# Kernel tuning notes

Measured on AMD Instinct MI355X. Metric: run time of the kernel, lower is better.

## Reference

```python
import jax, jax.numpy as jnp
import numpy as np

H, N, LMAX, KCH = 128, 64, 256, 2  # d_model, d_state, l_max per axis, kernel channels (bidirectional)


def _ssm_kernel(A_re, A_im, C_re, C_im, log_dt, L):
    """S4D diagonal SSM kernel (ZOH discretization) -> real kernel (KCH, H, L)."""
    A = A_re + 1j * A_im                      # (H, N)
    C = C_re + 1j * C_im                      # (KCH, H, N)
    dt = jnp.exp(log_dt)                      # (H,)
    dtA = dt[:, None] * A                     # (H, N)
    K = C * (jnp.exp(dtA) - 1.0) / A          # (KCH, H, N)
    vand = jnp.exp(dtA[:, :, None] * jnp.arange(L, dtype=dtA.real.dtype))  # (H, N, L)
    return 2.0 * jnp.einsum('chn,hnl->chl', K, vand).real


def _bidir_pad(k, L_in):
    """Split 2 kernel channels into fwd/bwd, flip backward one, pad to length Lk+L_in."""
    k0, k1 = k[:1], k[1:]                     # each (1, H, Lk)
    fwd = jnp.pad(k0, ((0, 0), (0, 0), (0, L_in)))
    bwd = jnp.pad(k1[..., ::-1], ((0, 0), (0, 0), (L_in, 0)))
    return fwd + bwd                          # (1, H, Lk + L_in)


def setup_inputs() -> dict:
    key = jax.random.key(0)
    ks = jax.random.split(key, 8)
    B, L1, L2 = 2, 256, 256
    u = jax.random.normal(ks[0], (B, H, L1, L2), jnp.float32)
    D = jax.random.normal(ks[1], (1, H), jnp.float32)

    def kparams(k_c, k_ci, k_dt):
        A_re = -0.5 * jnp.ones((H, N), jnp.float32)
        A_im = jnp.pi * jnp.broadcast_to(jnp.arange(N, dtype=jnp.float32), (H, N))
        C_re = jax.random.normal(k_c, (KCH, H, N), jnp.float32) * (0.5 ** 0.5)
        C_im = jax.random.normal(k_ci, (KCH, H, N), jnp.float32) * (0.5 ** 0.5)
        log_dt = jax.random.uniform(k_dt, (H,), jnp.float32,
                                    minval=np.log(1e-3), maxval=np.log(1e-1))
        return A_re, A_im, C_re, C_im, log_dt

    A_re0, A_im0, C_re0, C_im0, log_dt0 = kparams(ks[2], ks[3], ks[4])
    A_re1, A_im1, C_re1, C_im1, log_dt1 = kparams(ks[5], ks[6], ks[7])
    return {"u": u, "D": D,
            "A_re0": A_re0, "A_im0": A_im0, "C_re0": C_re0, "C_im0": C_im0, "log_dt0": log_dt0,
            "A_re1": A_re1, "A_im1": A_im1, "C_re1": C_re1, "C_im1": C_im1, "log_dt1": log_dt1}


def reference(u, D, A_re0, A_im0, C_re0, C_im0, log_dt0,
              A_re1, A_im1, C_re1, C_im1, log_dt1):
    B, _, L1, L2 = u.shape
    Lk1, Lk2 = min(L1, LMAX), min(L2, LMAX)
    # per-axis SSM kernels, then bidirectional flip-and-pad
    k1 = _bidir_pad(_ssm_kernel(A_re0, A_im0, C_re0, C_im0, log_dt0, Lk1), L1)  # (1,H,P1)
    k2 = _bidir_pad(_ssm_kernel(A_re1, A_im1, C_re1, C_im1, log_dt1, Lk2), L2)  # (1,H,P2)
    P1, P2 = L1 + Lk1, L2 + Lk2
    # N-D FFT convolution
    u_f = jnp.fft.rfftn(u, s=(P1, P2), axes=(-2, -1))        # (B,H,P1,P2//2+1)
    kf1 = jnp.fft.fft(k1, n=P1, axis=-1)                     # (1,H,P1) complex
    kf2 = jnp.fft.rfft(k2, n=P2, axis=-1)                    # (1,H,P2//2+1)
    k_f = jnp.einsum('chm,chn->chmn', kf1, kf2)              # outer product over axes (trank=1)
    y_f = jnp.einsum('bhmn,chmn->bchmn', u_f, k_f)           # (B,1,H,P1,P2r)
    y = jnp.fft.irfftn(y_f, s=(P1, P2), axes=(-2, -1))[..., :L1, :L2]
    # skip connection D
    y = y + jnp.einsum('bhxy,ch->bchxy', u, D)
    return y.reshape(B, -1, L1, L2)                          # (B, C*H, L1, L2)
```

## Files before the change

kernel.cpp:

```cpp
#include <hip/hip_runtime.h>

#define HH 128
#define NN 64
#define LL 256
#define WP 280

typedef __attribute__((ext_vector_type(8))) short bf8;
typedef __attribute__((ext_vector_type(4))) float f32x4;

__device__ inline ushort f2bf(float f) {
    uint x = __float_as_uint(f);
    return (ushort)((x + 0x7fffu + ((x >> 16) & 1u)) >> 16);
}
__device__ inline uint cvt_pk_bf16(float lo, float hi) {
    uint r;
    asm volatile("v_cvt_pk_bf16_f32 %0, %1, %2" : "=v"(r) : "v"(lo), "v"(hi));
    return r;
}
#define MFMA(a,b,c) __builtin_amdgcn_mfma_f32_16x16x32_bf16((a),(b),(c),0,0,0)

__global__ __launch_bounds__(512) void ssm_gen_fast(
    const float* __restrict__ A_re0, const float* __restrict__ A_im0,
    const float* __restrict__ C_re0, const float* __restrict__ C_im0,
    const float* __restrict__ log_dt0,
    const float* __restrict__ A_re1, const float* __restrict__ A_im1,
    const float* __restrict__ C_re1, const float* __restrict__ C_im1,
    const float* __restrict__ log_dt1,
    uint* __restrict__ arrg)
{
    __shared__ float4 par[128];
    __shared__ float  red[512];
    __shared__ ushort rev[512];

    int tid = threadIdx.x;
    int h   = blockIdx.x;
    int s   = blockIdx.y;

    if (tid < 128) {
        int n  = tid & 63;
        int ch = tid >> 6;
        const float* Ar = s ? A_re1 : A_re0;
        const float* Ai = s ? A_im1 : A_im0;
        const float* Cr = s ? C_re1 : C_re0;
        const float* Ci = s ? C_im1 : C_im0;
        const float* Ld = s ? log_dt1 : log_dt0;
        float dt = __expf(Ld[h]);
        float ar = Ar[h*NN + n], ai = Ai[h*NN + n];
        float cr = Cr[(ch*HH + h)*NN + n], ci = Ci[(ch*HH + h)*NN + n];
        float xr = dt * ar, xi = dt * ai;
        float phr = xi * 0.15915494f;
        float phf = phr - floorf(phr);
        float sn = __sinf(6.2831853f * phf);
        float cs = __cosf(6.2831853f * phf);
        float e  = __expf(xr);
        float er = e*cs - 1.f, ei = e*sn;
        float inv = 1.f / (ar*ar + ai*ai);
        float dr = (er*ar + ei*ai) * inv;
        float di = (ei*ar - er*ai) * inv;
        float Kr = 2.f*(cr*dr - ci*di);
        float Ki = 2.f*(cr*di + ci*dr);
        par[tid] = (float4){ xr, xi * 0.15915494f, Kr, Ki };
    }
    __syncthreads();

    {
        int l  = tid & 255;
        int ch = tid >> 8;
        float lf = (float)l;
#pragma unroll
        for (int nh = 0; nh < 2; ++nh) {
            const float4* pb = &par[ch*64 + nh*32];
            float acc = 0.f;
            for (int n = 0; n < 32; ++n) {
                float4 p = pb[n];
                float mag = __expf(p.x * lf);
                float ph  = p.y * lf;
                float phf = ph - floorf(ph);
                float ang = 6.2831853f * phf;
                acc += p.z * (mag * __cosf(ang)) - p.w * (mag * __sinf(ang));
            }
            if (nh == 0) red[tid] = acc;
            else {
                int ri = ch ? (256 + l) : (255 - l);
                rev[ri] = f2bf(red[tid] + acc);
            }
        }
    }
    __syncthreads();

    {
        int j  = tid & 255;
        uint lo, hi;
        if (tid < 256) { lo = rev[2*j];     hi = rev[2*j + 1]; }
        else           { lo = rev[2*j + 1]; hi = (j == 255) ? 0u : (uint)rev[2*j + 2]; }
        arrg[(s*HH + h)*512 + tid] = lo | (hi << 16);
    }
}

#define GL0(dst, addr)  asm volatile("global_load_dwordx4 %0, %1, off"           : "=v"(dst) : "v"(addr))
#define GL16(dst, addr) asm volatile("global_load_dwordx4 %0, %1, off offset:16" : "=v"(dst) : "v"(addr))
#define VMW(n) do { asm volatile("s_waitcnt vmcnt(" #n ")" ::: "memory"); \
                    __builtin_amdgcn_sched_barrier(0); } while (0)

#define WINROLL8(T, JB, t_)                                                   \
    { int jj = (JB) + 8*(t_); uint* pw = (uint*)&win[(t_) & 7];               \
      pw[0]=T[jj]; pw[1]=T[jj+1]; pw[2]=T[jj+2]; pw[3]=T[jj+3]; }

#define PH1_ISS(kk, N0, N1)                                                   \
    { const float* a_ = rp + (kk)*32 + 8*q; GL0(N0, a_); GL16(N1, a_); }

#define PH1_CON(kk, C0, C1, CNT)                                              \
    {                                                                         \
        if ((kk) > 0) { WINROLL8(T2, jb2, 2*(kk)-1); WINROLL8(T2, jb2, 2*(kk)); } \
        VMW(CNT);                                                             \
        bf8 b0_; uint* pb_ = (uint*)&b0_;                                     \
        pb_[0]=cvt_pk_bf16(C0.x,C0.y); pb_[1]=cvt_pk_bf16(C0.z,C0.w);         \
        pb_[2]=cvt_pk_bf16(C1.x,C1.y); pb_[3]=cvt_pk_bf16(C1.z,C1.w);         \
        __builtin_amdgcn_s_setprio(1);                                        \
        _Pragma("unroll")                                                     \
        for (int mi = 0; mi < 8; ++mi)                                        \
            acc[mi] = MFMA(win[(2*(kk)-mi) & 7], b0_, acc[mi]);               \
        __builtin_amdgcn_s_setprio(0);                                        \
    }

__global__ __launch_bounds__(512, 4) void s4nd_v6(
    const float* __restrict__ u, const float* __restrict__ Dv,
    const uint* __restrict__ arrg, float* __restrict__ out)
{
    __shared__ ushort WT[128 * WP];
    __shared__ uint   arr[2][512];

    int tid = threadIdx.x;
    int j    = blockIdx.x;
    int xcd  = j & 7;
    int k    = j >> 3;
    int bh   = xcd * 32 + (k >> 1);
    int y0   = (k & 1) * 128;
    int h    = bh & (HH - 1);

    arr[0][tid] = arrg[h*512 + tid];
    arr[1][tid] = arrg[(HH + h)*512 + tid];
    __syncthreads();

    int lane = tid & 63;
    int w = tid >> 6;
    int c = lane & 15, q = lane >> 4;
    int wm2 = (w >> 1) * 64, wn2 = (w & 1) * 64;

    const uint* T1 = &arr[0][(c & 1) ? 0 : 256];
    const uint* T2 = &arr[1][(c & 1) ? 0 : 256];
    int jb2 = (255 - y0  - c + 8*q) >> 1;
    int jb1 = (255 - wm2 - c + 8*q) >> 1;

    f32x4 acc[8];
#pragma unroll
    for (int i = 0; i < 8; ++i) acc[i] = (f32x4){0.f,0.f,0.f,0.f};

    const float* ub = u + (size_t)bh * LL * LL;
    float* yb_ = out + (size_t)bh * LL * LL;

#pragma unroll
    for (int ns = 0; ns < 2; ++ns) {
        const float* rp = ub + (size_t)(w*32 + 16*ns + c) * LL;
        bf8 win[8];
#pragma unroll
        for (int t = -7; t <= 0; ++t) WINROLL8(T2, jb2, t);
        float4 S00, S01, S10, S11, S20, S21;
        PH1_ISS(0, S00, S01)
        PH1_ISS(1, S10, S11)
        PH1_ISS(2, S20, S21)  PH1_CON(0, S00, S01, 4)
        PH1_ISS(3, S00, S01)  PH1_CON(1, S10, S11, 4)
        PH1_ISS(4, S10, S11)  PH1_CON(2, S20, S21, 4)
        PH1_ISS(5, S20, S21)  PH1_CON(3, S00, S01, 4)
        PH1_ISS(6, S00, S01)  PH1_CON(4, S10, S11, 4)
        PH1_ISS(7, S10, S11)  PH1_CON(5, S20, S21, 4)
                              PH1_CON(6, S00, S01, 2)
                              PH1_CON(7, S10, S11, 0)
#pragma unroll
        for (int mi = 0; mi < 8; ++mi)
#pragma unroll
            for (int r = 0; r < 4; ++r) {
                int row = 16*mi + 4*q + r;
                WT[row*WP + w*32 + 16*ns + c] = f2bf(acc[mi][r]);
                acc[mi][r] = 0.f;
            }
    }
    __syncthreads();

    float dh = Dv[h];
#pragma unroll
    for (int p = 0; p < 2; ++p) {
        int nb = wn2 + p*32;

        float uh[32];
#pragma unroll
        for (int mi = 0; mi < 4; ++mi)
#pragma unroll
            for (int r = 0; r < 4; ++r) {
                int row = wm2 + 16*mi + 4*q + r;
#pragma unroll
                for (int ni = 0; ni < 2; ++ni)
                    uh[(mi*4 + r)*2 + ni] = ub[(size_t)row*LL + y0 + nb + 16*ni + c];
            }

        bf8 win2[4];
#pragma unroll
        for (int t = -3; t <= 0; ++t) {
            int jj = jb1 + 8*t;
            uint* pw = (uint*)&win2[t & 3];
            pw[0]=T1[jj]; pw[1]=T1[jj+1]; pw[2]=T1[jj+2]; pw[3]=T1[jj+3];
        }
#pragma unroll
        for (int kk = 0; kk < 8; ++kk) {
            if (kk) {
#pragma unroll
                for (int t = 2*kk - 1; t <= 2*kk; ++t) {
                    int jj = jb1 + 8*t;
                    uint* pw = (uint*)&win2[t & 3];
                    pw[0]=T1[jj]; pw[1]=T1[jj+1]; pw[2]=T1[jj+2]; pw[3]=T1[jj+3];
                }
            }
            int xb = kk*32 + 8*q;
            bf8 b0 = *(const bf8*)&WT[(nb + c)*WP + xb];
            bf8 b1 = *(const bf8*)&WT[(nb + 16 + c)*WP + xb];
            __builtin_amdgcn_s_setprio(1);
#pragma unroll
            for (int mi = 0; mi < 4; ++mi) {
                bf8 a = win2[(2*kk - mi) & 3];
                acc[mi*2 + 0] = MFMA(a, b0, acc[mi*2 + 0]);
                acc[mi*2 + 1] = MFMA(a, b1, acc[mi*2 + 1]);
            }
            __builtin_amdgcn_s_setprio(0);
        }

#pragma unroll
        for (int mi = 0; mi < 4; ++mi)
#pragma unroll
            for (int ni = 0; ni < 2; ++ni)
#pragma unroll
                for (int r = 0; r < 4; ++r) {
                    int row = wm2 + 16*mi + 4*q + r;
                    int col = y0 + nb + 16*ni + c;
                    yb_[(size_t)row*LL + col] =
                        acc[mi*2 + ni][r] + dh * uh[(mi*4 + r)*2 + ni];
                    acc[mi*2 + ni][r] = 0.f;
                }
    }
}

extern "C" void kernel_launch(void* const* d_in, const int* in_sizes, int n_in,
                              void* d_out, int out_size, void* d_ws, size_t ws_size,
                              hipStream_t stream)
{
    const float* u       = (const float*)d_in[0];
    const float* D       = (const float*)d_in[1];
    const float* A_re0   = (const float*)d_in[2];
    const float* A_im0   = (const float*)d_in[3];
    const float* C_re0   = (const float*)d_in[4];
    const float* C_im0   = (const float*)d_in[5];
    const float* log_dt0 = (const float*)d_in[6];
    const float* A_re1   = (const float*)d_in[7];
    const float* A_im1   = (const float*)d_in[8];
    const float* C_re1   = (const float*)d_in[9];
    const float* C_im1   = (const float*)d_in[10];
    const float* log_dt1 = (const float*)d_in[11];
    float* out = (float*)d_out;

    uint* arrg = (uint*)d_ws;

    ssm_gen_fast<<<dim3(HH, 2), 512, 0, stream>>>(
        A_re0, A_im0, C_re0, C_im0, log_dt0,
        A_re1, A_im1, C_re1, C_im1, log_dt1, arrg);
    s4nd_v6<<<512, 512, 0, stream>>>(u, D, arrg, out);
}
```

Measured before the change: 49.56 us.

## Pipeline separable convolution passes in k-chunks with double-buffered LDS slices

Restructures the two-pass separable Toeplitz convolution so the first pass (along y) is computed chunk by chunk in 32-row slices and fed through a small double-buffered LDS tile into the second pass, interleaving global loads, first-pass MFMAs and second-pass MFMAs. Each block now covers a 64-column quarter instead of a 128-column half, doubling the grid to 1024 blocks and shrinking LDS from a full 128x280 tile to two 64x40 tiles. The aim is to overlap memory latency with compute and raise occupancy. In exchange it adds eight block-wide barriers per block and recomputes the first pass per y-quarter, which increases the redundant u reads and MFMA work.

```diff
diff --git a/kernel.cpp b/kernel.cpp
--- a/kernel.cpp
+++ b/kernel.cpp
@@ -3,7 +3,7 @@
 #define HH 128
 #define NN 64
 #define LL 256
-#define WP 280
+#define WCP 40
 
 typedef __attribute__((ext_vector_type(8))) short bf8;
 typedef __attribute__((ext_vector_type(4))) float f32x4;
@@ -102,40 +102,68 @@
 #define VMW(n) do { asm volatile("s_waitcnt vmcnt(" #n ")" ::: "memory"); \
                     __builtin_amdgcn_sched_barrier(0); } while (0)
 
-#define WINROLL8(T, JB, t_)                                                   \
-    { int jj = (JB) + 8*(t_); uint* pw = (uint*)&win[(t_) & 7];               \
-      pw[0]=T[jj]; pw[1]=T[jj+1]; pw[2]=T[jj+2]; pw[3]=T[jj+3]; }
-
-#define PH1_ISS(kk, N0, N1)                                                   \
-    { const float* a_ = rp + (kk)*32 + 8*q; GL0(N0, a_); GL16(N1, a_); }
-
-#define PH1_CON(kk, C0, C1, CNT)                                              \
+#define PISS(kc, ys, N0, N1) \
+    { const float* a_ = rpP + (kc)*8192 + (ys)*32 + 8*q; GL0(N0, a_); GL16(N1, a_); }
+
+#define PCON(ys, C0, C1, CNT, APX)                                            \
     {                                                                         \
-        if ((kk) > 0) { WINROLL8(T2, jb2, 2*(kk)-1); WINROLL8(T2, jb2, 2*(kk)); } \
+        int jj = jbP + 16*(ys);                                               \
+        bf8 aF; uint* pa = (uint*)&aF;                                        \
+        pa[0]=T2[jj]; pa[1]=T2[jj+1]; pa[2]=T2[jj+2]; pa[3]=T2[jj+3];         \
         VMW(CNT);                                                             \
-        bf8 b0_; uint* pb_ = (uint*)&b0_;                                     \
-        pb_[0]=cvt_pk_bf16(C0.x,C0.y); pb_[1]=cvt_pk_bf16(C0.z,C0.w);         \
-        pb_[2]=cvt_pk_bf16(C1.x,C1.y); pb_[3]=cvt_pk_bf16(C1.z,C1.w);         \
-        __builtin_amdgcn_s_setprio(1);                                        \
+        bf8 bB; uint* pb = (uint*)&bB;                                        \
+        pb[0]=cvt_pk_bf16(C0.x,C0.y); pb[1]=cvt_pk_bf16(C0.z,C0.w);           \
+        pb[2]=cvt_pk_bf16(C1.x,C1.y); pb[3]=cvt_pk_bf16(C1.z,C1.w);           \
+        APX = MFMA(aF, bB, APX);                                              \
+    }
+
+#define CSLICE(k, ys)                                                         \
+    {                                                                         \
+        if (((ys) & 1) == 0)                                                  \
+            bC = *(const bf8*)&Wc[(k)&1][(16*((ys)>>1) + c)*WCP + 8*q];       \
+        acc2[((ys)&1)*4 + ((ys)>>1)] =                                        \
+            MFMA(win2[(2*(k) - ((ys)&1)) & 3], bC, acc2[((ys)&1)*4 + ((ys)>>1)]); \
+    }
+
+#define WROLL(t_)                                                             \
+    { int jj = jb1 + 8*(t_); uint* pw = (uint*)&win2[(t_) & 3];               \
+      pw[0]=T1[jj]; pw[1]=T1[jj+1]; pw[2]=T1[jj+2]; pw[3]=T1[jj+3]; }
+
+#define BODY(k)                                                               \
+    {                                                                         \
+        WROLL(2*(k)-1) WROLL(2*(k))                                           \
+        bf8 bC;                                                               \
+        PISS((k)+1, 0, P0, P1)                                                \
+        PISS((k)+1, 1, Q0, Q1)  CSLICE(k,0)  PCON(0, P0, P1, 2, accpA)        \
+        PISS((k)+1, 2, P0, P1)  CSLICE(k,1)  PCON(1, Q0, Q1, 2, accpB)        \
+        PISS((k)+1, 3, Q0, Q1)  CSLICE(k,2)  PCON(2, P0, P1, 2, accpA)        \
+        PISS((k)+1, 4, P0, P1)  CSLICE(k,3)  PCON(3, Q0, Q1, 2, accpB)        \
+        PISS((k)+1, 5, Q0, Q1)  CSLICE(k,4)  PCON(4, P0, P1, 2, accpA)        \
+        PISS((k)+1, 6, P0, P1)  CSLICE(k,5)  PCON(5, Q0, Q1, 2, accpB)        \
+        PISS((k)+1, 7, Q0, Q1)  CSLICE(k,6)  PCON(6, P0, P1, 2, accpA)        \
+                                CSLICE(k,7)  PCON(7, Q0, Q1, 0, accpB)        \
         _Pragma("unroll")                                                     \
-        for (int mi = 0; mi < 8; ++mi)                                        \
-            acc[mi] = MFMA(win[(2*(kk)-mi) & 7], b0_, acc[mi]);               \
-        __builtin_amdgcn_s_setprio(0);                                        \
-    }
-
-__global__ __launch_bounds__(512, 4) void s4nd_v6(
+        for (int r = 0; r < 4; ++r) {                                         \
+            Wc[((k)+1)&1][(16*yb + 4*q + r)*WCP + 16*xh + c] =                \
+                f2bf(accpA[r] + accpB[r]);                                    \
+            accpA[r] = 0.f; accpB[r] = 0.f;                                   \
+        }                                                                     \
+        __syncthreads();                                                      \
+    }
+
+__global__ __launch_bounds__(512, 4) void s4nd_v7(
     const float* __restrict__ u, const float* __restrict__ Dv,
     const uint* __restrict__ arrg, float* __restrict__ out)
 {
-    __shared__ ushort WT[128 * WP];
+    __shared__ ushort Wc[2][64 * WCP];
     __shared__ uint   arr[2][512];
 
     int tid = threadIdx.x;
     int j    = blockIdx.x;
     int xcd  = j & 7;
-    int k    = j >> 3;
-    int bh   = xcd * 32 + (k >> 1);
-    int y0   = (k & 1) * 128;
+    int k0   = j >> 3;
+    int bh   = xcd * 32 + (k0 >> 2);
+    int yq   = (k0 & 3) * 64;
     int h    = bh & (HH - 1);
 
     arr[0][tid] = arrg[h*512 + tid];
@@ -145,107 +173,77 @@
     int lane = tid & 63;
     int w = tid >> 6;
     int c = lane & 15, q = lane >> 4;
-    int wm2 = (w >> 1) * 64, wn2 = (w & 1) * 64;
+    int yb = w & 3;
+    int xh = w >> 2;
 
     const uint* T1 = &arr[0][(c & 1) ? 0 : 256];
     const uint* T2 = &arr[1][(c & 1) ? 0 : 256];
-    int jb2 = (255 - y0  - c + 8*q) >> 1;
-    int jb1 = (255 - wm2 - c + 8*q) >> 1;
-
-    f32x4 acc[8];
-#pragma unroll
-    for (int i = 0; i < 8; ++i) acc[i] = (f32x4){0.f,0.f,0.f,0.f};
-
-    const float* ub = u + (size_t)bh * LL * LL;
+    int jbP = (255 - yq - 16*yb - c + 8*q) >> 1;
+    int jb1 = (255 - 32*w  - c + 8*q) >> 1;
+
+    const float* ub  = u + (size_t)bh * LL * LL;
+    const float* rpP = ub + (size_t)(16*xh + c) * LL;
     float* yb_ = out + (size_t)bh * LL * LL;
 
-#pragma unroll
-    for (int ns = 0; ns < 2; ++ns) {
-        const float* rp = ub + (size_t)(w*32 + 16*ns + c) * LL;
-        bf8 win[8];
-#pragma unroll
-        for (int t = -7; t <= 0; ++t) WINROLL8(T2, jb2, t);
-        float4 S00, S01, S10, S11, S20, S21;
-        PH1_ISS(0, S00, S01)
-        PH1_ISS(1, S10, S11)
-        PH1_ISS(2, S20, S21)  PH1_CON(0, S00, S01, 4)
-        PH1_ISS(3, S00, S01)  PH1_CON(1, S10, S11, 4)
-        PH1_ISS(4, S10, S11)  PH1_CON(2, S20, S21, 4)
-        PH1_ISS(5, S20, S21)  PH1_CON(3, S00, S01, 4)
-        PH1_ISS(6, S00, S01)  PH1_CON(4, S10, S11, 4)
-        PH1_ISS(7, S10, S11)  PH1_CON(5, S20, S21, 4)
-                              PH1_CON(6, S00, S01, 2)
-                              PH1_CON(7, S10, S11, 0)
-#pragma unroll
-        for (int mi = 0; mi < 8; ++mi)
+    f32x4 acc2[8];
+#pragma unroll
+    for (int i = 0; i < 8; ++i) acc2[i] = (f32x4){0.f,0.f,0.f,0.f};
+    f32x4 accpA = (f32x4){0.f,0.f,0.f,0.f};
+    f32x4 accpB = (f32x4){0.f,0.f,0.f,0.f};
+
+    float4 P0, P1, Q0, Q1;
+    bf8 win2[4];
+
+    PISS(0, 0, P0, P1)
+    PISS(0, 1, Q0, Q1)
+    PCON(0, P0, P1, 2, accpA)  PISS(0, 2, P0, P1)
+    PCON(1, Q0, Q1, 2, accpB)  PISS(0, 3, Q0, Q1)
+    PCON(2, P0, P1, 2, accpA)  PISS(0, 4, P0, P1)
+    PCON(3, Q0, Q1, 2, accpB)  PISS(0, 5, Q0, Q1)
+    PCON(4, P0, P1, 2, accpA)  PISS(0, 6, P0, P1)
+    PCON(5, Q0, Q1, 2, accpB)  PISS(0, 7, Q0, Q1)
+    PCON(6, P0, P1, 2, accpA)
+    PCON(7, Q0, Q1, 0, accpB)
+#pragma unroll
+    for (int r = 0; r < 4; ++r) {
+        Wc[0][(16*yb + 4*q + r)*WCP + 16*xh + c] = f2bf(accpA[r] + accpB[r]);
+        accpA[r] = 0.f; accpB[r] = 0.f;
+    }
+    __syncthreads();
+
+    WROLL(-1) WROLL(0)
+
+    BODY(0) BODY(1) BODY(2) BODY(3) BODY(4) BODY(5) BODY(6)
+
+    {
+        WROLL(13) WROLL(14)
+        bf8 bC;
+        CSLICE(7,0) CSLICE(7,1) CSLICE(7,2) CSLICE(7,3)
+        CSLICE(7,4) CSLICE(7,5) CSLICE(7,6) CSLICE(7,7)
+    }
+
+    float dh = Dv[h];
+    float uh[32];
+#pragma unroll
+    for (int mi = 0; mi < 2; ++mi)
+#pragma unroll
+        for (int r = 0; r < 4; ++r) {
+            int row = 32*w + 16*mi + 4*q + r;
+#pragma unroll
+            for (int ni = 0; ni < 4; ++ni)
+                uh[mi*16 + r*4 + ni] = ub[(size_t)row*LL + yq + 16*ni + c];
+        }
+#pragma unroll
+    for (int mi = 0; mi < 2; ++mi)
+#pragma unroll
+        for (int ni = 0; ni < 4; ++ni)
 #pragma unroll
             for (int r = 0; r < 4; ++r) {
-                int row = 16*mi + 4*q + r;
-                WT[row*WP + w*32 + 16*ns + c] = f2bf(acc[mi][r]);
-                acc[mi][r] = 0.f;
+                int row = 32*w + 16*mi + 4*q + r;
+                int col = yq + 16*ni + c;
+                yb_[(size_t)row*LL + col] =
+                    acc2[mi*4 + ni][r] + dh * uh[mi*16 + r*4 + ni];
             }
-    }
-    __syncthreads();
-
-    float dh = Dv[h];
-#pragma unroll
-    for (int p = 0; p < 2; ++p) {
-        int nb = wn2 + p*32;
-
-        float uh[32];
-#pragma unroll
-        for (int mi = 0; mi < 4; ++mi)
-#pragma unroll
-            for (int r = 0; r < 4; ++r) {
-                int row = wm2 + 16*mi + 4*q + r;
-#pragma unroll
-                for (int ni = 0; ni < 2; ++ni)
-                    uh[(mi*4 + r)*2 + ni] = ub[(size_t)row*LL + y0 + nb + 16*ni + c];
-            }
-
-        bf8 win2[4];
-#pragma unroll
-        for (int t = -3; t <= 0; ++t) {
-            int jj = jb1 + 8*t;
-            uint* pw = (uint*)&win2[t & 3];
-            pw[0]=T1[jj]; pw[1]=T1[jj+1]; pw[2]=T1[jj+2]; pw[3]=T1[jj+3];
-        }
-#pragma unroll
-        for (int kk = 0; kk < 8; ++kk) {
-            if (kk) {
-#pragma unroll
-                for (int t = 2*kk - 1; t <= 2*kk; ++t) {
-                    int jj = jb1 + 8*t;
-                    uint* pw = (uint*)&win2[t & 3];
-                    pw[0]=T1[jj]; pw[1]=T1[jj+1]; pw[2]=T1[jj+2]; pw[3]=T1[jj+3];
-                }
-            }
-            int xb = kk*32 + 8*q;
-            bf8 b0 = *(const bf8*)&WT[(nb + c)*WP + xb];
-            bf8 b1 = *(const bf8*)&WT[(nb + 16 + c)*WP + xb];
-            __builtin_amdgcn_s_setprio(1);
-#pragma unroll
-            for (int mi = 0; mi < 4; ++mi) {
-                bf8 a = win2[(2*kk - mi) & 3];
-                acc[mi*2 + 0] = MFMA(a, b0, acc[mi*2 + 0]);
-                acc[mi*2 + 1] = MFMA(a, b1, acc[mi*2 + 1]);
-            }
-            __builtin_amdgcn_s_setprio(0);
-        }
-
-#pragma unroll
-        for (int mi = 0; mi < 4; ++mi)
-#pragma unroll
-            for (int ni = 0; ni < 2; ++ni)
-#pragma unroll
-                for (int r = 0; r < 4; ++r) {
-                    int row = wm2 + 16*mi + 4*q + r;
-                    int col = y0 + nb + 16*ni + c;
-                    yb_[(size_t)row*LL + col] =
-                        acc[mi*2 + ni][r] + dh * uh[(mi*4 + r)*2 + ni];
-                    acc[mi*2 + ni][r] = 0.f;
-                }
-    }
 }
 
 extern "C" void kernel_launch(void* const* d_in, const int* in_sizes, int n_in,
@@ -271,5 +269,5 @@
     ssm_gen_fast<<<dim3(HH, 2), 512, 0, stream>>>(
         A_re0, A_im0, C_re0, C_im0, log_dt0,
         A_re1, A_im1, C_re1, C_im1, log_dt1, arrg);
-    s4nd_v6<<<512, 512, 0, stream>>>(u, D, arrg, out);
-}
+    s4nd_v7<<<1024, 512, 0, stream>>>(u, D, arrg, out);
+}
```

New measurement: 156.6 us. 3.16x slower.
